# Kernel tuning notes

Hardware: AMD Instinct MI355X
Metric: run time of the kernel (lower is better)

Reference implementation:

```python
import jax, jax.numpy as jnp
import numpy as np

BOX = 256           # box_size
OS = 2              # grid_oversampling_factor
GRID = BOX * OS     # oversampled image size
NPTS = 30000        # n_points
NCLS = 2            # n_classes
NLAT = 16           # n_latent_dims
NLAY = 6            # n_layers
H = 256             # n_neurons_per_layer
L = 10              # pos_enc_dim
BATCH = 4


def positional_encoding(pos, n_freq):
    # NeRF-style: sin/cos(2^k * pi * x) per coordinate -> [N, 6*n_freq]
    freqs = 2.0 ** jnp.arange(n_freq, dtype=pos.dtype)
    ang = pos[..., None] * freqs * jnp.pi                    # [N,3,L]
    enc = jnp.concatenate([jnp.sin(ang), jnp.cos(ang)], axis=-1)
    return enc.reshape(pos.shape[0], 6 * n_freq)


def euler_zyz_to_matrix(ang):
    # ang: [B,3] -> R = Rz(a) @ Ry(b) @ Rz(c), [B,3,3]
    a, b, c = ang[:, 0], ang[:, 1], ang[:, 2]
    ca, sa = jnp.cos(a), jnp.sin(a)
    cb, sb = jnp.cos(b), jnp.sin(b)
    cc, sc = jnp.cos(c), jnp.sin(c)
    row0 = jnp.stack([ca * cb * cc - sa * sc, -ca * cb * sc - sa * cc, ca * sb], -1)
    row1 = jnp.stack([sa * cb * cc + ca * sc, -sa * cb * sc + ca * cc, sa * sb], -1)
    row2 = jnp.stack([-sb * cc, sb * sc, cb], -1)
    return jnp.stack([row0, row1, row2], axis=-2)


def points_to_images(proj, amps):
    # proj: [B,N,2] in [-0.5,0.5]; amps: [B,C,N] -> [B,C,GRID,GRID] via bilinear splat
    B, N, _ = proj.shape
    C = amps.shape[1]
    p = jnp.clip((proj + 0.5) * (GRID - 1), 0.0, GRID - 1.000001)
    x, y = p[..., 0], p[..., 1]
    x0f = jnp.floor(x); y0f = jnp.floor(y)
    fx = x - x0f; fy = y - y0f
    x0 = x0f.astype(jnp.int32); y0 = y0f.astype(jnp.int32)
    x1 = jnp.minimum(x0 + 1, GRID - 1); y1 = jnp.minimum(y0 + 1, GRID - 1)
    w = jnp.stack([(1 - fx) * (1 - fy), fx * (1 - fy), (1 - fx) * fy, fx * fy], -1)  # [B,N,4]
    xi = jnp.stack([x0, x1, x0, x1], -1)
    yi = jnp.stack([y0, y0, y1, y1], -1)
    pix = yi * GRID + xi                                            # [B,N,4]
    bc = (jnp.arange(B)[:, None] * C + jnp.arange(C)[None, :])      # [B,C]
    idx = bc[:, :, None, None] * (GRID * GRID) + pix[:, None, :, :]  # [B,C,N,4]
    vals = amps[:, :, :, None] * w[:, None, :, :]                    # [B,C,N,4]
    img = jnp.zeros((B * C * GRID * GRID,), vals.dtype)
    img = img.at[idx.reshape(-1)].add(vals.reshape(-1))
    return img.reshape(B, C, GRID, GRID)


def fourier_smooth(images, A, B_width):
    # per-class Gaussian low-pass in Fourier, sum classes, crop oversampled grid to BOX
    f = jnp.fft.fftfreq(GRID).astype(images.dtype)
    R = f[None, :] ** 2 + f[:, None] ** 2                            # [G,G]
    filt = A[:, None, None] * jnp.exp(-(B_width[:, None, None] ** 2) * R)
    F = jnp.fft.fft2(images)                                         # [B,C,G,G]
    Fs = jnp.sum(filt * F, axis=1)                                   # [B,G,G]
    Fs = jnp.fft.fftshift(Fs, axes=(-2, -1))
    s = (GRID - BOX) // 2
    Fc = Fs[:, s:s + BOX, s:s + BOX]
    Fc = jnp.fft.ifftshift(Fc, axes=(-2, -1))
    return jnp.real(jnp.fft.ifft2(Fc)) / (OS * OS)


def fourier_shift_2d(im, sx, sy):
    f = jnp.fft.fftfreq(BOX)
    phase = jnp.exp(-2j * jnp.pi * (sx[:, None, None] * f[None, None, :]
                                    + sy[:, None, None] * f[None, :, None]))
    return jnp.real(jnp.fft.ifft2(jnp.fft.fft2(im) * phase))


def setup_inputs() -> dict:
    key = jax.random.key(0)
    ks = jax.random.split(key, 10)
    din = 6 * L + NLAT
    return {
        "z": jax.random.normal(ks[0], (BATCH, NLAT), jnp.float32),
        "orientation": jax.random.uniform(ks[1], (BATCH, 3), jnp.float32, 0.0, 2.0 * np.pi),
        "shift": jax.random.normal(ks[2], (BATCH, 2), jnp.float32) * 2.0,
        "model_positions": jax.random.uniform(ks[3], (NPTS, 3), jnp.float32, -0.4, 0.4),
        "amp": 50.0 * jnp.ones((NCLS, NPTS), jnp.float32),
        "ampvar": jax.random.normal(ks[4], (NCLS, NPTS), jnp.float32),
        "W_in": jax.random.normal(ks[5], (din, H), jnp.float32) / np.sqrt(din),
        "W_layers": jax.random.normal(ks[6], (NLAY, H, H), jnp.float32) / np.sqrt(H),
        "W_out1": jax.random.normal(ks[7], (H, 3), jnp.float32) / np.sqrt(H),
        "W_out2": jax.random.normal(ks[8], (3, 3), jnp.float32) * 0.01,
        "A": jnp.ones((NCLS,), jnp.float32),
        "B_width": 5.0 * jnp.ones((NCLS,), jnp.float32),
    }


def reference(z, orientation, shift, model_positions, amp, ampvar,
              W_in, W_layers, W_out1, W_out2, A, B_width):
    B = z.shape[0]
    # --- displacement MLP (mask=None, warmup=False path) ---
    enc = positional_encoding(model_positions, L)                    # [N,6L]
    feat = jnp.concatenate([
        jnp.broadcast_to(enc[None], (B, NPTS, 6 * L)),
        jnp.broadcast_to(z[:, None, :], (B, NPTS, NLAT)),
    ], axis=-1)                                                      # [B,N,6L+lat]
    h = feat @ W_in                                                  # input Linear (no bias)
    for i in range(NLAY):                                            # LinearBlock = ELU(Linear)
        h = jax.nn.elu(h @ W_layers[i])
    disp = jax.nn.elu(h @ W_out1) @ W_out2                           # [B,N,3]
    final_pos = model_positions[None] + disp                         # [B,N,3]
    # --- projection ---
    Rm = euler_zyz_to_matrix(orientation)                            # [B,3,3]
    proj = jnp.einsum('bnd,bde->bne', final_pos, Rm)[..., :2]        # [B,N,2]
    # --- amplitudes, splat, smooth, shift ---
    wamp = amp * jax.nn.softmax(ampvar, axis=0)                      # [C,N]
    wamp = jnp.broadcast_to(wamp[None], (B, NCLS, NPTS))
    imgs = points_to_images(proj, wamp)                              # [B,C,G,G]
    sm = fourier_smooth(imgs, A, B_width)                            # [B,BOX,BOX]
    out = fourier_shift_2d(sm, shift[:, 0], shift[:, 1])
    return out, final_pos, disp
```

## Files before the change

### kernel.cpp

```cpp
#include <hip/hip_runtime.h>

#define PI_F 3.14159265358979323846f

constexpr int GRIDN = 512;
constexpr int BOXN  = 256;
constexpr int NPTS  = 30000;
constexpr int NCLS  = 2;
constexpr int NLAT  = 16;
constexpr int HDIM  = 256;
constexpr int LFREQ = 10;
constexpr int BATCH = 4;
constexpr int NROWS = BATCH*NPTS;
constexpr int RM    = 48;

#define ASC   2048.0f
#define AINV  (1.0f/2048.0f)
#define OINV  (1.0f/33554432.0f)
#define BSC   16384.0f

typedef _Float16 f16x8 __attribute__((ext_vector_type(8)));
typedef float    f32x4 __attribute__((ext_vector_type(4)));

__device__ __forceinline__ float elu_f(float x){ return x > 0.f ? x : (__expf(x) - 1.0f); }

__device__ __forceinline__ void split_f16(float vs, uint32_t& hb, uint32_t& lb){
    const _Float16 h = (_Float16)vs;
    const _Float16 l = (_Float16)(vs - (float)h);
    union { _Float16 f; uint16_t u; } uh, ul;
    uh.f = h; ul.f = l;
    hb = uh.u; lb = ul.u;
}
__device__ __forceinline__ uint32_t pack_act(float v){
    uint32_t hb, lb;
    split_f16(v * ASC, hb, lb);
    return hb | (lb << 16);
}
__device__ __forceinline__ float unpack_act(uint32_t u){
    union { uint16_t u16; _Float16 f; } a, b;
    a.u16 = (uint16_t)(u & 0xffffu);
    b.u16 = (uint16_t)(u >> 16);
    return ((float)a.f + (float)b.f) * AINV;
}

__host__ __device__ __forceinline__ size_t wp_off(int lay){
    return (lay == 0) ? 0 : (size_t)(98304 + (lay-1)*262144);
}

__global__ void prepack_kernel(const float* __restrict__ Win,
                               const float* __restrict__ Wlay,
                               unsigned char* __restrict__ wp)
{
    const int tid = blockIdx.x*256 + threadIdx.x;
    if (tid >= 7*8*16*64) return;
    const int lane  = tid & 63;
    const int n16   = (tid >> 6) & 15;
    const int kstep = (tid >> 10) & 7;
    const int lay   = tid >> 13;
    if (lay == 0 && kstep >= 3) return;
    const int kbase = 32*kstep + 8*(lane >> 4);
    const int c = 16*n16 + (lane & 15);
    uint32_t hw[4], lw[4];
    #pragma unroll
    for (int p = 0; p < 4; ++p) {
        uint32_t hh0=0, hh1=0, ll0=0, ll1=0;
        #pragma unroll
        for (int q = 0; q < 2; ++q) {
            const int k = kbase + 2*p + q;
            float w = 0.f;
            if (lay == 0) { if (k < 76) w = Win[k*HDIM + c]; }
            else w = Wlay[(size_t)(lay-1)*HDIM*HDIM + (size_t)k*HDIM + c];
            uint32_t hb, lb;
            split_f16(w * BSC, hb, lb);
            if (q == 0) { hh0 = hb; ll0 = lb; } else { hh1 = hb; ll1 = lb; }
        }
        hw[p] = hh0 | (hh1 << 16);
        lw[p] = ll0 | (ll1 << 16);
    }
    uint4* dst = (uint4*)(wp + wp_off(lay)) + (size_t)((kstep*16 + n16)*2)*64 + lane;
    dst[0]  = make_uint4(hw[0], hw[1], hw[2], hw[3]);
    dst[64] = make_uint4(lw[0], lw[1], lw[2], lw[3]);
}

__launch_bounds__(512, 4)
__global__ void mlp_fused(const float* __restrict__ pos,
                          const float* __restrict__ zlat,
                          const unsigned char* __restrict__ wp,
                          const float* __restrict__ Wout1,
                          const float* __restrict__ Wout2,
                          const float* __restrict__ orient,
                          float* __restrict__ out_fp,
                          float* __restrict__ out_disp,
                          float2* __restrict__ proj)
{
    __shared__ uint4 h4[RM*64];
    __shared__ float w1s[HDIM*3];
    uint32_t* hs = (uint32_t*)h4;
    const int t = threadIdx.x;
    const int lane = t & 63;
    const int wv = t >> 6;
    const int row0 = blockIdx.x * RM;
    const int g  = lane >> 4;
    const int rb = lane & 15;

    for (int idx = t; idx < RM*96; idx += 512) {
        const int r = idx / 96, c = idx - r*96;
        const int row = row0 + r;
        const int b = row / NPTS, n = row - b*NPTS;
        float v = 0.f;
        if (c < 60) {
            const int d = c / 20, rem = c - d*20;
            const int f = (rem < 10) ? rem : rem - 10;
            const float ang = pos[n*3+d] * (float)(1<<f) * PI_F;
            v = (rem < 10) ? sinf(ang) : cosf(ang);
        } else if (c < 76) {
            v = zlat[b*NLAT + (c - 60)];
        }
        hs[r*256 + (c ^ ((r&7)<<2))] = pack_act(v);
    }
    for (int idx = t; idx < HDIM*3; idx += 512) w1s[idx] = Wout1[idx];
    __syncthreads();

    for (int lay = 0; lay < 7; ++lay) {
        const int KS = lay ? 8 : 3;
        const uint4* bp = (const uint4*)(wp + wp_off(lay));

        f32x4 acc[6];
        #pragma unroll
        for (int i = 0; i < 6; ++i) { f32x4 zz = {0.f,0.f,0.f,0.f}; acc[i] = zz; }

        uint4 BH0[2], BL0[2], BH1[2], BL1[2];

        auto LOADB = [&](uint4 (&H)[2], uint4 (&L)[2], int k){
            #pragma unroll
            for (int f = 0; f < 2; ++f) {
                const size_t s0 = (size_t)((k*16 + 2*wv + f)*2)*64 + lane;
                H[f] = bp[s0];
                L[f] = bp[s0 + 64];
            }
        };
        auto STEP = [&](const uint4 (&H)[2], const uint4 (&L)[2], int k){
            #pragma unroll
            for (int m = 0; m < 3; ++m) {
                const int r = 16*m + rb;
                const int s = r & 7;
                const int G0 = 8*k + 2*g;
                const uint4 p0 = h4[r*64 + (G0 ^ s)];
                const uint4 p1 = h4[r*64 + ((G0+1) ^ s)];
                const uint32_t e0=p0.x, e1=p0.y, e2=p0.z, e3=p0.w;
                const uint32_t e4=p1.x, e5=p1.y, e6=p1.z, e7=p1.w;
                union { uint4 q; f16x8 v; } ah, al;
                ah.q = make_uint4((e0 & 0xffffu) | (e1 << 16),
                                  (e2 & 0xffffu) | (e3 << 16),
                                  (e4 & 0xffffu) | (e5 << 16),
                                  (e6 & 0xffffu) | (e7 << 16));
                al.q = make_uint4((e0 >> 16) | (e1 & 0xffff0000u),
                                  (e2 >> 16) | (e3 & 0xffff0000u),
                                  (e4 >> 16) | (e5 & 0xffff0000u),
                                  (e6 >> 16) | (e7 & 0xffff0000u));
                #pragma unroll
                for (int nn = 0; nn < 2; ++nn) {
                    union { uint4 q; f16x8 v; } bh, bl;
                    bh.q = H[nn]; bl.q = L[nn];
                    f32x4 a = acc[m*2+nn];
                    a = __builtin_amdgcn_mfma_f32_16x16x32_f16(ah.v, bl.v, a, 0, 0, 0);
                    a = __builtin_amdgcn_mfma_f32_16x16x32_f16(al.v, bh.v, a, 0, 0, 0);
                    a = __builtin_amdgcn_mfma_f32_16x16x32_f16(ah.v, bh.v, a, 0, 0, 0);
                    acc[m*2+nn] = a;
                }
            }
        };

        LOADB(BH0, BL0, 0);
        for (int k = 0; k < KS; k += 2) {
            if (k+1 < KS) LOADB(BH1, BL1, k+1);
            STEP(BH0, BL0, k);
            if (k+1 < KS) {
                if (k+2 < KS) LOADB(BH0, BL0, k+2);
                STEP(BH1, BL1, k+1);
            }
        }

        __syncthreads();
        const bool do_elu = (lay >= 1);
        #pragma unroll
        for (int m = 0; m < 3; ++m) {
            #pragma unroll
            for (int nn = 0; nn < 2; ++nn) {
                #pragma unroll
                for (int j = 0; j < 4; ++j) {
                    float v = acc[m*2+nn][j] * OINV;
                    if (do_elu) v = elu_f(v);
                    const int r = 16*m + 4*g + j;
                    const int c = 32*wv + 16*nn + rb;
                    hs[r*256 + (c ^ ((r&7)<<2))] = pack_act(v);
                }
            }
        }
        __syncthreads();
    }

    if (t < RM) {
        const int row = row0 + t;
        const int b = row / NPTS, n = row - b*NPTS;
        const int s = (t & 7) << 2;
        float o0=0.f, o1=0.f, o2=0.f;
        for (int k = 0; k < HDIM; ++k) {
            const float hv = unpack_act(hs[t*256 + (k ^ s)]);
            o0 = fmaf(hv, w1s[k*3+0], o0);
            o1 = fmaf(hv, w1s[k*3+1], o1);
            o2 = fmaf(hv, w1s[k*3+2], o2);
        }
        o0 = elu_f(o0); o1 = elu_f(o1); o2 = elu_f(o2);
        const float d0 = o0*Wout2[0] + o1*Wout2[3] + o2*Wout2[6];
        const float d1 = o0*Wout2[1] + o1*Wout2[4] + o2*Wout2[7];
        const float d2 = o0*Wout2[2] + o1*Wout2[5] + o2*Wout2[8];
        const float p0 = pos[n*3+0] + d0;
        const float p1 = pos[n*3+1] + d1;
        const float p2 = pos[n*3+2] + d2;
        out_disp[(size_t)row*3+0] = d0; out_disp[(size_t)row*3+1] = d1; out_disp[(size_t)row*3+2] = d2;
        out_fp[(size_t)row*3+0]   = p0; out_fp[(size_t)row*3+1]   = p1; out_fp[(size_t)row*3+2]   = p2;
        float sa,ca,sb,cb,sc,cc;
        sincosf(orient[b*3+0], &sa, &ca);
        sincosf(orient[b*3+1], &sb, &cb);
        sincosf(orient[b*3+2], &sc, &cc);
        const float R00 =  ca*cb*cc - sa*sc;
        const float R10 =  sa*cb*cc + ca*sc;
        const float R20 = -sb*cc;
        const float R01 = -ca*cb*sc - sa*cc;
        const float R11 = -sa*cb*sc + ca*cc;
        const float R21 =  sb*sc;
        float2 pr;
        pr.x = p0*R00 + p1*R10 + p2*R20;
        pr.y = p0*R01 + p1*R11 + p2*R21;
        proj[row] = pr;
    }
}

__global__ void scatter_kernel(const float2* __restrict__ proj,
                               const float* __restrict__ amp,
                               const float* __restrict__ ampvar,
                               float* __restrict__ img)
{
    const int i = blockIdx.x * 256 + threadIdx.x;
    if (i >= NROWS) return;
    const int b = i / NPTS;
    const int n = i - b*NPTS;
    const float2 pr = proj[i];
    float x = (pr.x + 0.5f) * (float)(GRIDN-1);
    float y = (pr.y + 0.5f) * (float)(GRIDN-1);
    x = fminf(fmaxf(x, 0.f), 511.0f);
    y = fminf(fmaxf(y, 0.f), 511.0f);
    const float x0f = floorf(x), y0f = floorf(y);
    const float fx = x - x0f, fy = y - y0f;
    const int x0 = (int)x0f, y0 = (int)y0f;
    const int x1 = min(x0+1, GRIDN-1), y1 = min(y0+1, GRIDN-1);
    const float av0 = ampvar[n], av1 = ampvar[NPTS + n];
    const float m  = fmaxf(av0, av1);
    const float e0 = __expf(av0 - m), e1 = __expf(av1 - m);
    const float inv = 1.0f / (e0 + e1);
    const float w0 = amp[n]        * e0 * inv;
    const float w1 = amp[NPTS + n] * e1 * inv;
    const float w00 = (1.f-fx)*(1.f-fy), w10 = fx*(1.f-fy), w01 = (1.f-fx)*fy, w11 = fx*fy;
    float* img0 = img + (size_t)(b*NCLS + 0)*GRIDN*GRIDN;
    float* img1 = img + (size_t)(b*NCLS + 1)*GRIDN*GRIDN;
    const int i00 = y0*GRIDN + x0, i10 = y0*GRIDN + x1;
    const int i01 = y1*GRIDN + x0, i11 = y1*GRIDN + x1;
    atomicAdd(img0 + i00, w0*w00); atomicAdd(img0 + i10, w0*w10);
    atomicAdd(img0 + i01, w0*w01); atomicAdd(img0 + i11, w0*w11);
    atomicAdd(img1 + i00, w1*w00); atomicAdd(img1 + i10, w1*w10);
    atomicAdd(img1 + i01, w1*w01); atomicAdd(img1 + i11, w1*w11);
}

__global__ void fft_row_pair(const float* __restrict__ img, float2* __restrict__ Z)
{
    __shared__ float2 s[512];
    const int t  = threadIdx.x;
    const int rb = blockIdx.x;
    const int b  = rb >> 9, y = rb & 511;
    const float* p0 = img + ((size_t)(b*2+0) << 18) + (size_t)y*512;
    const float* p1 = img + ((size_t)(b*2+1) << 18) + (size_t)y*512;
    #pragma unroll
    for (int j = 0; j < 2; ++j) {
        const int i  = t + j*256;
        const int ri = (int)(__brev((unsigned)i) >> 23);
        s[ri] = make_float2(p0[i], p1[i]);
    }
    for (int len = 1; len < 512; len <<= 1) {
        __syncthreads();
        const int p  = t & (len-1);
        const int i0 = ((t & ~(len-1)) << 1) | p;
        const float ang = -PI_F * (float)p / (float)len;
        float sn, cs; __sincosf(ang, &sn, &cs);
        const float2 a  = s[i0];
        const float2 bv = s[i0 + len];
        const float2 bt = make_float2(bv.x*cs - bv.y*sn, bv.x*sn + bv.y*cs);
        s[i0]       = make_float2(a.x + bt.x, a.y + bt.y);
        s[i0 + len] = make_float2(a.x - bt.x, a.y - bt.y);
    }
    __syncthreads();
    float2* zo = Z + ((size_t)b << 18) + (size_t)y*512;
    #pragma unroll
    for (int j = 0; j < 2; ++j) {
        const int i = t + j*256;
        zo[i] = s[i];
    }
}

template<int N, bool INV, bool RIN, bool ROUT>
__global__ void fft_pass(const float* __restrict__ in, float* __restrict__ out,
                         int in_per, long in_s1, long in_s2, long in_es,
                         int out_per, long out_s1, long out_s2, long out_es,
                         float scale)
{
    __shared__ float2 s[N];
    const int t  = threadIdx.x;
    const int rb = blockIdx.x;
    const long ib = (long)(rb / in_per) * in_s1 + (long)(rb % in_per) * in_s2;
    constexpr int LOG2N = (N == 512) ? 9 : 8;
    #pragma unroll
    for (int j = 0; j < 2; ++j) {
        const int i  = t + j*(N/2);
        const int ri = (int)(__brev((unsigned)i) >> (32 - LOG2N));
        float2 v;
        if (RIN) { v.x = in[ib + (long)i*in_es]; v.y = 0.f; }
        else       v = ((const float2*)in)[ib + (long)i*in_es];
        s[ri] = v;
    }
    for (int len = 1; len < N; len <<= 1) {
        __syncthreads();
        const int p  = t & (len-1);
        const int i0 = ((t & ~(len-1)) << 1) | p;
        const float ang = (INV ? PI_F : -PI_F) * (float)p / (float)len;
        float sn, cs; __sincosf(ang, &sn, &cs);
        const float2 a  = s[i0];
        const float2 bv = s[i0 + len];
        const float2 bt = make_float2(bv.x*cs - bv.y*sn, bv.x*sn + bv.y*cs);
        s[i0]       = make_float2(a.x + bt.x, a.y + bt.y);
        s[i0 + len] = make_float2(a.x - bt.x, a.y - bt.y);
    }
    __syncthreads();
    const long ob = (long)(rb / out_per) * out_s1 + (long)(rb % out_per) * out_s2;
    #pragma unroll
    for (int j = 0; j < 2; ++j) {
        const int i = t + j*(N/2);
        if (ROUT) out[ob + (long)i*out_es] = s[i].x * scale;
        else {
            float2 v = s[i]; v.x *= scale; v.y *= scale;
            ((float2*)out)[ob + (long)i*out_es] = v;
        }
    }
}

__global__ void combine_kernel(const float2* __restrict__ Z,
                               const float* __restrict__ Afac,
                               const float* __restrict__ Bw,
                               const float* __restrict__ shift,
                               float2* __restrict__ Q)
{
    const int u = blockIdx.x;
    const int b = blockIdx.y;
    const int v = threadIdx.x;
    const int mu  = (u < 128) ? u : u + 256;
    const int mv  = (v < 128) ? v : v + 256;
    const int u2  = (256 - u) & 255;
    const int v2  = (256 - v) & 255;
    const int mu2 = (u2 < 128) ? u2 : u2 + 256;
    const int mv2 = (v2 < 128) ? v2 : v2 + 256;
    const int nmu  = (512 - mu)  & 511;
    const int nmv  = (512 - mv)  & 511;
    const int nmu2 = (512 - mu2) & 511;
    const int nmv2 = (512 - mv2) & 511;

    const float2* Zb = Z + ((size_t)b << 18);
    const float2 A   = Zb[(size_t)mu  *512 + mv ];
    const float2 Am  = Zb[(size_t)nmu *512 + nmv];
    const float2 A2  = Zb[(size_t)mu2 *512 + mv2];
    const float2 A2m = Zb[(size_t)nmu2*512 + nmv2];

    float2 F1v[2], FHv[2];
    F1v[0] = make_float2(0.5f*(A.x + Am.x),  0.5f*(A.y - Am.y));
    F1v[1] = make_float2(0.5f*(A.y + Am.y), -0.5f*(A.x - Am.x));
    FHv[0] = make_float2(0.5f*(A2.x + A2m.x),  0.5f*(A2.y - A2m.y));
    FHv[1] = make_float2(0.5f*(A2.y + A2m.y), -0.5f*(A2.x - A2m.x));

    const float fy1 = (float)((mu  < 256) ? mu  : mu  - 512) / 512.0f;
    const float fx1 = (float)((mv  < 256) ? mv  : mv  - 512) / 512.0f;
    const float fy2 = (float)((mu2 < 256) ? mu2 : mu2 - 512) / 512.0f;
    const float fx2 = (float)((mv2 < 256) ? mv2 : mv2 - 512) / 512.0f;
    const float R1 = fy1*fy1 + fx1*fx1;
    const float R2 = fy2*fy2 + fx2*fx2;
    float a1x=0.f, a1y=0.f, a2x=0.f, a2y=0.f;
    #pragma unroll
    for (int c = 0; c < NCLS; ++c) {
        const float bw = Bw[c];
        const float f1 = Afac[c] * __expf(-bw*bw*R1);
        const float f2 = Afac[c] * __expf(-bw*bw*R2);
        a1x = fmaf(f1, F1v[c].x, a1x); a1y = fmaf(f1, F1v[c].y, a1y);
        a2x = fmaf(f2, FHv[c].x, a2x); a2y = fmaf(f2, FHv[c].y, a2y);
    }
    const float Gx = 0.5f*(a1x + a2x);
    const float Gy = 0.5f*(a1y - a2y);
    const float fu = (float)((u < 128) ? u : u - 256) / 256.0f;
    const float fv = (float)((v < 128) ? v : v - 256) / 256.0f;
    const float th = -2.0f*PI_F*(shift[b*2+0]*fv + shift[b*2+1]*fu);
    float sn, cs; __sincosf(th, &sn, &cs);
    float2 o;
    o.x = Gx*cs - Gy*sn;
    o.y = Gx*sn + Gy*cs;
    Q[((size_t)b << 16) + (size_t)u*256 + v] = o;
}

extern "C" void kernel_launch(void* const* d_in, const int* in_sizes, int n_in,
                              void* d_out, int out_size, void* d_ws, size_t ws_size,
                              hipStream_t stream)
{
    (void)in_sizes; (void)n_in; (void)out_size; (void)ws_size;
    const float* z      = (const float*)d_in[0];
    const float* orient = (const float*)d_in[1];
    const float* shift  = (const float*)d_in[2];
    const float* pos    = (const float*)d_in[3];
    const float* amp    = (const float*)d_in[4];
    const float* ampvar = (const float*)d_in[5];
    const float* Win    = (const float*)d_in[6];
    const float* Wlay   = (const float*)d_in[7];
    const float* Wout1  = (const float*)d_in[8];
    const float* Wout2  = (const float*)d_in[9];
    const float* Afac   = (const float*)d_in[10];
    const float* Bw     = (const float*)d_in[11];

    float* out      = (float*)d_out;
    float* out_img  = out;
    float* out_fp   = out + (size_t)BATCH*BOXN*BOXN;
    float* out_disp = out_fp + (size_t)NROWS*3;

    char*   ws   = (char*)d_ws;
    float*  img  = (float*)ws;
    float2* Zb   = (float2*)(ws + (size_t)8*1024*1024);
    unsigned char* wp = (unsigned char*)(ws + (size_t)8*1024*1024);
    float2* Q    = (float2*)(ws + (size_t)25165824);
    float2* proj = (float2*)(ws + (size_t)27262976);

    (void)hipMemsetAsync(img, 0, (size_t)BATCH*NCLS*GRIDN*GRIDN*sizeof(float), stream);

    prepack_kernel<<<(7*8*16*64 + 255)/256, 256, 0, stream>>>(Win, Wlay, wp);

    mlp_fused<<<NROWS/RM, 512, 0, stream>>>(pos, z, wp, Wout1, Wout2, orient,
                                            out_fp, out_disp, proj);
    scatter_kernel<<<(NROWS+255)/256, 256, 0, stream>>>(proj, amp, ampvar, img);

    fft_row_pair<<<BATCH*512, 256, 0, stream>>>(img, Zb);
    fft_pass<512,false,false,false><<<BATCH*512, 256, 0, stream>>>(
        (const float*)Zb, (float*)Zb, 512, 262144, 1, 512, 512, 262144, 1, 512, 1.0f);

    combine_kernel<<<dim3(256, BATCH), 256, 0, stream>>>(Zb, Afac, Bw, shift, Q);

    fft_pass<256,true ,false,false><<<BATCH*256, 128, 0, stream>>>(
        (const float*)Q, (float*)Q, 256, 65536, 256, 1, 256, 65536, 256, 1, 1.0f/256.0f);
    fft_pass<256,true ,false,true ><<<BATCH*256, 128, 0, stream>>>(
        (const float*)Q, out_img, 256, 65536, 1, 256, 256, 65536, 1, 256, 0.25f/256.0f);
}
```

Before: 482.7 us.

## Fuse bilinear splat into MLP epilogue and parallelize output head across four lanes

The separate scatter kernel is removed and its softmax-weighted bilinear atomic splat runs directly in the MLP kernel's epilogue, so the intermediate projection buffer is no longer written and read back and one launch is dropped. The final 256-to-3 dot product now splits each row across four threads and combines the partial sums with cross-lane shuffles, where before one thread per row walked all 256 terms. Atomics are now issued from the MLP blocks, and only a quarter of the threads in each block do the tail work.

```diff
diff --git a/kernel.cpp b/kernel.cpp
--- a/kernel.cpp
+++ b/kernel.cpp
@@ -88,9 +88,11 @@
                           const float* __restrict__ Wout1,
                           const float* __restrict__ Wout2,
                           const float* __restrict__ orient,
+                          const float* __restrict__ amp,
+                          const float* __restrict__ ampvar,
                           float* __restrict__ out_fp,
                           float* __restrict__ out_disp,
-                          float2* __restrict__ proj)
+                          float* __restrict__ img)
 {
     __shared__ uint4 h4[RM*64];
     __shared__ float w1s[HDIM*3];
@@ -199,76 +201,75 @@
         __syncthreads();
     }
 
-    if (t < RM) {
-        const int row = row0 + t;
-        const int b = row / NPTS, n = row - b*NPTS;
-        const int s = (t & 7) << 2;
-        float o0=0.f, o1=0.f, o2=0.f;
-        for (int k = 0; k < HDIM; ++k) {
-            const float hv = unpack_act(hs[t*256 + (k ^ s)]);
-            o0 = fmaf(hv, w1s[k*3+0], o0);
-            o1 = fmaf(hv, w1s[k*3+1], o1);
-            o2 = fmaf(hv, w1s[k*3+2], o2);
-        }
-        o0 = elu_f(o0); o1 = elu_f(o1); o2 = elu_f(o2);
-        const float d0 = o0*Wout2[0] + o1*Wout2[3] + o2*Wout2[6];
-        const float d1 = o0*Wout2[1] + o1*Wout2[4] + o2*Wout2[7];
-        const float d2 = o0*Wout2[2] + o1*Wout2[5] + o2*Wout2[8];
-        const float p0 = pos[n*3+0] + d0;
-        const float p1 = pos[n*3+1] + d1;
-        const float p2 = pos[n*3+2] + d2;
-        out_disp[(size_t)row*3+0] = d0; out_disp[(size_t)row*3+1] = d1; out_disp[(size_t)row*3+2] = d2;
-        out_fp[(size_t)row*3+0]   = p0; out_fp[(size_t)row*3+1]   = p1; out_fp[(size_t)row*3+2]   = p2;
-        float sa,ca,sb,cb,sc,cc;
-        sincosf(orient[b*3+0], &sa, &ca);
-        sincosf(orient[b*3+1], &sb, &cb);
-        sincosf(orient[b*3+2], &sc, &cc);
-        const float R00 =  ca*cb*cc - sa*sc;
-        const float R10 =  sa*cb*cc + ca*sc;
-        const float R20 = -sb*cc;
-        const float R01 = -ca*cb*sc - sa*cc;
-        const float R11 = -sa*cb*sc + ca*cc;
-        const float R21 =  sb*sc;
-        float2 pr;
-        pr.x = p0*R00 + p1*R10 + p2*R20;
-        pr.y = p0*R01 + p1*R11 + p2*R21;
-        proj[row] = pr;
-    }
-}
-
-__global__ void scatter_kernel(const float2* __restrict__ proj,
-                               const float* __restrict__ amp,
-                               const float* __restrict__ ampvar,
-                               float* __restrict__ img)
-{
-    const int i = blockIdx.x * 256 + threadIdx.x;
-    if (i >= NROWS) return;
-    const int b = i / NPTS;
-    const int n = i - b*NPTS;
-    const float2 pr = proj[i];
-    float x = (pr.x + 0.5f) * (float)(GRIDN-1);
-    float y = (pr.y + 0.5f) * (float)(GRIDN-1);
-    x = fminf(fmaxf(x, 0.f), 511.0f);
-    y = fminf(fmaxf(y, 0.f), 511.0f);
-    const float x0f = floorf(x), y0f = floorf(y);
-    const float fx = x - x0f, fy = y - y0f;
-    const int x0 = (int)x0f, y0 = (int)y0f;
-    const int x1 = min(x0+1, GRIDN-1), y1 = min(y0+1, GRIDN-1);
-    const float av0 = ampvar[n], av1 = ampvar[NPTS + n];
-    const float m  = fmaxf(av0, av1);
-    const float e0 = __expf(av0 - m), e1 = __expf(av1 - m);
-    const float inv = 1.0f / (e0 + e1);
-    const float w0 = amp[n]        * e0 * inv;
-    const float w1 = amp[NPTS + n] * e1 * inv;
-    const float w00 = (1.f-fx)*(1.f-fy), w10 = fx*(1.f-fy), w01 = (1.f-fx)*fy, w11 = fx*fy;
-    float* img0 = img + (size_t)(b*NCLS + 0)*GRIDN*GRIDN;
-    float* img1 = img + (size_t)(b*NCLS + 1)*GRIDN*GRIDN;
-    const int i00 = y0*GRIDN + x0, i10 = y0*GRIDN + x1;
-    const int i01 = y1*GRIDN + x0, i11 = y1*GRIDN + x1;
-    atomicAdd(img0 + i00, w0*w00); atomicAdd(img0 + i10, w0*w10);
-    atomicAdd(img0 + i01, w0*w01); atomicAdd(img0 + i11, w0*w11);
-    atomicAdd(img1 + i00, w1*w00); atomicAdd(img1 + i10, w1*w10);
-    atomicAdd(img1 + i01, w1*w01); atomicAdd(img1 + i11, w1*w11);
+    {
+        const int r = t >> 2;
+        const int q = t & 3;
+        if (r < RM) {
+            const int s = (r & 7) << 2;
+            const uint32_t* hr = hs + r*256;
+            float o0=0.f, o1=0.f, o2=0.f;
+            #pragma unroll 8
+            for (int kk = 0; kk < 64; ++kk) {
+                const int k = 64*q + kk;
+                const float hv = unpack_act(hr[k ^ s]);
+                o0 = fmaf(hv, w1s[k*3+0], o0);
+                o1 = fmaf(hv, w1s[k*3+1], o1);
+                o2 = fmaf(hv, w1s[k*3+2], o2);
+            }
+            o0 += __shfl_xor(o0, 1); o0 += __shfl_xor(o0, 2);
+            o1 += __shfl_xor(o1, 1); o1 += __shfl_xor(o1, 2);
+            o2 += __shfl_xor(o2, 1); o2 += __shfl_xor(o2, 2);
+            if (q == 0) {
+                const int row = row0 + r;
+                const int b = row / NPTS, n = row - b*NPTS;
+                o0 = elu_f(o0); o1 = elu_f(o1); o2 = elu_f(o2);
+                const float d0 = o0*Wout2[0] + o1*Wout2[3] + o2*Wout2[6];
+                const float d1 = o0*Wout2[1] + o1*Wout2[4] + o2*Wout2[7];
+                const float d2 = o0*Wout2[2] + o1*Wout2[5] + o2*Wout2[8];
+                const float p0 = pos[n*3+0] + d0;
+                const float p1 = pos[n*3+1] + d1;
+                const float p2 = pos[n*3+2] + d2;
+                out_disp[(size_t)row*3+0] = d0; out_disp[(size_t)row*3+1] = d1; out_disp[(size_t)row*3+2] = d2;
+                out_fp[(size_t)row*3+0]   = p0; out_fp[(size_t)row*3+1]   = p1; out_fp[(size_t)row*3+2]   = p2;
+                float sa,ca,sb,cb,sc,cc;
+                sincosf(orient[b*3+0], &sa, &ca);
+                sincosf(orient[b*3+1], &sb, &cb);
+                sincosf(orient[b*3+2], &sc, &cc);
+                const float R00 =  ca*cb*cc - sa*sc;
+                const float R10 =  sa*cb*cc + ca*sc;
+                const float R20 = -sb*cc;
+                const float R01 = -ca*cb*sc - sa*cc;
+                const float R11 = -sa*cb*sc + ca*cc;
+                const float R21 =  sb*sc;
+                const float prx = p0*R00 + p1*R10 + p2*R20;
+                const float pry = p0*R01 + p1*R11 + p2*R21;
+
+                float x = (prx + 0.5f) * (float)(GRIDN-1);
+                float y = (pry + 0.5f) * (float)(GRIDN-1);
+                x = fminf(fmaxf(x, 0.f), 511.0f);
+                y = fminf(fmaxf(y, 0.f), 511.0f);
+                const float x0f = floorf(x), y0f = floorf(y);
+                const float fx = x - x0f, fy = y - y0f;
+                const int x0 = (int)x0f, y0 = (int)y0f;
+                const int x1 = min(x0+1, GRIDN-1), y1 = min(y0+1, GRIDN-1);
+                const float av0 = ampvar[n], av1 = ampvar[NPTS + n];
+                const float mx = fmaxf(av0, av1);
+                const float e0 = __expf(av0 - mx), e1 = __expf(av1 - mx);
+                const float inv = 1.0f / (e0 + e1);
+                const float w0 = amp[n]        * e0 * inv;
+                const float w1 = amp[NPTS + n] * e1 * inv;
+                const float w00 = (1.f-fx)*(1.f-fy), w10 = fx*(1.f-fy), w01 = (1.f-fx)*fy, w11 = fx*fy;
+                float* img0 = img + (size_t)(b*NCLS + 0)*GRIDN*GRIDN;
+                float* img1 = img + (size_t)(b*NCLS + 1)*GRIDN*GRIDN;
+                const int i00 = y0*GRIDN + x0, i10 = y0*GRIDN + x1;
+                const int i01 = y1*GRIDN + x0, i11 = y1*GRIDN + x1;
+                atomicAdd(img0 + i00, w0*w00); atomicAdd(img0 + i10, w0*w10);
+                atomicAdd(img0 + i01, w0*w01); atomicAdd(img0 + i11, w0*w11);
+                atomicAdd(img1 + i00, w1*w00); atomicAdd(img1 + i10, w1*w10);
+                atomicAdd(img1 + i01, w1*w01); atomicAdd(img1 + i11, w1*w11);
+            }
+        }
+    }
 }
 
 __global__ void fft_row_pair(const float* __restrict__ img, float2* __restrict__ Z)
@@ -438,15 +439,13 @@
     float2* Zb   = (float2*)(ws + (size_t)8*1024*1024);
     unsigned char* wp = (unsigned char*)(ws + (size_t)8*1024*1024);
     float2* Q    = (float2*)(ws + (size_t)25165824);
-    float2* proj = (float2*)(ws + (size_t)27262976);
 
     (void)hipMemsetAsync(img, 0, (size_t)BATCH*NCLS*GRIDN*GRIDN*sizeof(float), stream);
 
     prepack_kernel<<<(7*8*16*64 + 255)/256, 256, 0, stream>>>(Win, Wlay, wp);
 
     mlp_fused<<<NROWS/RM, 512, 0, stream>>>(pos, z, wp, Wout1, Wout2, orient,
-                                            out_fp, out_disp, proj);
-    scatter_kernel<<<(NROWS+255)/256, 256, 0, stream>>>(proj, amp, ampvar, img);
+                                            amp, ampvar, out_fp, out_disp, img);
 
     fft_row_pair<<<BATCH*512, 256, 0, stream>>>(img, Zb);
     fft_pass<512,false,false,false><<<BATCH*512, 256, 0, stream>>>(
```

New measurement: 427.0 us, median of 2. -11.5%, faster.
